# Optimization experiments

Measured on AMD Instinct MI355X. Metric: run time of the kernel, lower is better.

The kernel has to match this reference:

```python
import jax, jax.numpy as jnp
import numpy as np

NUM_PIECES = 32

def _conv(x, w, pad):
    # NCHW conv, stride 1
    return jax.lax.conv_general_dilated(x, w, (1, 1), [(pad, pad), (pad, pad)],
                                        dimension_numbers=('NCHW', 'OIHW', 'NCHW'))

def _bn(x, s, b):
    # eval-mode BatchNorm folded to per-channel affine (running mean/var folded into s,b)
    return x * s[None, :, None, None] + b[None, :, None, None]

def setup_inputs() -> dict:
    key = jax.random.key(0)
    ks = jax.random.split(key, 24)
    N, CIN, H, W = 1024, 13, 8, 8
    C = 64          # final conv channels
    S, NB = 7, 7    # stages, conv blocks per stage
    P = NUM_PIECES
    feat = jax.random.normal(ks[0], (N, CIN - 1, H, W), jnp.float32)
    ids = jax.random.randint(ks[1], (N, 1, H, W), 0, P + 1).astype(jnp.float32)
    x = jnp.concatenate([feat, ids], axis=1)  # last channel = piece ids
    n = jax.random.normal
    inp = {
        'x': x,
        'first_w': n(ks[2], (C - 1, CIN - 1, 7, 7), jnp.float32) * 0.05,
        'first_s': 1.0 + 0.1 * n(ks[3], (C - 1,), jnp.float32),
        'first_b': 0.05 * n(ks[4], (C - 1,), jnp.float32),
        'res_w': n(ks[5], (S, NB, C, C, 7, 7), jnp.float32) * 0.02,
        'res_s': 1.0 + 0.1 * n(ks[6], (S, NB, C), jnp.float32),
        'res_b': 0.05 * n(ks[7], (S, NB, C), jnp.float32),
        'last_w': n(ks[8], (S, C, C), jnp.float32) * 0.05,
        'last_s': 1.0 + 0.1 * n(ks[9], (S, C), jnp.float32),
        'last_b': 0.05 * n(ks[10], (S, C), jnp.float32),
        'pfc1_w': n(ks[11], (256, P * C), jnp.float32) * 0.02,
        'pfc1_b': jnp.zeros((256,), jnp.float32),
        'pfc2_w': n(ks[12], (1700, 256), jnp.float32) * 0.02,
        'pfc2_b': jnp.zeros((1700,), jnp.float32),
        'vconv_w': n(ks[13], (1, C, 1, 1), jnp.float32) * 0.05,
        'v_s': 1.0 + 0.1 * n(ks[14], (1,), jnp.float32),
        'v_b': 0.05 * n(ks[15], (1,), jnp.float32),
        'vfc1_w': n(ks[16], (256, H * W), jnp.float32) * 0.02,
        'vfc1_b': jnp.zeros((256,), jnp.float32),
        'vfc2_w': n(ks[17], (1, 256), jnp.float32) * 0.02,
        'vfc2_b': jnp.zeros((1,), jnp.float32),
    }
    return inp

def reference(x, first_w, first_s, first_b, res_w, res_s, res_b, last_w, last_s, last_b,
              pfc1_w, pfc1_b, pfc2_w, pfc2_b, vconv_w, v_s, v_b,
              vfc1_w, vfc1_b, vfc2_w, vfc2_b):
    N = x.shape[0]
    P = NUM_PIECES
    conv_in = x[:, :-1]           # (N, 12, 8, 8)
    ids_f = x[:, -1]              # (N, 8, 8) float piece ids
    ids = ids_f.astype(jnp.int32)
    h = jax.nn.relu(_bn(_conv(conv_in, first_w, 3), first_s, first_b))  # (N, 63, 8, 8)
    conv_feat = jnp.concatenate([h, ids_f[:, None]], axis=1)            # (N, 64, 8, 8)
    # --- fused piece-vector extraction (replaces batch x piece torch.where loop) ---
    ids_flat = ids.reshape(N, -1)                                       # (N, 64)
    match = ids_flat[:, None, :] == jnp.arange(1, P + 1, dtype=jnp.int32)[None, :, None]  # (N,P,64)
    idx = jnp.argmax(match, axis=-1)                                    # first occurrence, row-major
    present = match.any(-1)
    board_t = conv_feat.reshape(N, conv_feat.shape[1], -1).transpose(0, 2, 1)  # (N, 64pos, C)
    piece_vec = jnp.take_along_axis(board_t, idx[:, :, None], axis=1)          # (N, P, C)
    piece_vec = piece_vec * present[:, :, None].astype(piece_vec.dtype)
    pid_hist = [piece_vec[:, :, -1][:, None, :]]
    S, NB = res_w.shape[0], res_w.shape[1]
    for i in range(S):
        h = conv_feat
        for j in range(NB):
            h = jax.nn.relu(_bn(_conv(h, res_w[i, j], 3), res_s[i, j], res_b[i, j]))
        h = _bn(jnp.einsum('nchw,oc->nohw', h, last_w[i]), last_s[i], last_b[i])  # 1x1 conv
        conv_feat = jax.nn.relu(h + conv_feat)
        pid_hist.append(piece_vec[:, :, -1][:, None, :])
    piece_ids_out = jnp.concatenate(pid_hist, axis=1)  # (N, S+1, P)
    # policy head
    hid = jax.nn.relu(piece_vec.reshape(N, -1) @ pfc1_w.T + pfc1_b)
    policy = hid @ pfc2_w.T + pfc2_b                   # (N, 1700)
    # value head
    v = jax.nn.relu(_bn(_conv(conv_feat, vconv_w, 0), v_s, v_b)).reshape(N, -1)  # (N, 64)
    v = jax.nn.relu(v @ vfc1_w.T + vfc1_b)
    value = jnp.tanh(v @ vfc2_w.T + vfc2_b)            # (N, 1)
    return (policy, value, piece_ids_out)
```

## Files before the change

### kernel.cpp

```cpp
#include <hip/hip_runtime.h>

typedef __attribute__((ext_vector_type(8)))  short          bf16x8;
typedef __attribute__((ext_vector_type(16))) float          f32x16;
typedef __attribute__((ext_vector_type(4)))  unsigned int   uint4v;
typedef __attribute__((ext_vector_type(4)))  unsigned short ushort4v;
typedef __attribute__((ext_vector_type(4)))  float          float4v;

#define DEV static __device__ __forceinline__
#define MFMA32(A,B,C) __builtin_amdgcn_mfma_f32_32x32x16_bf16(A,B,C,0,0,0)

#define WRES_OFF 0u
#define FW_OFF   9863168u
#define P1_OFF   9913344u
#define P2_OFF   10437632u
#define ACT0_OFF 10896384u
#define PV_OFF   15090688u
#define HID_OFF  17187840u

#define VAL_OFF 1740800
#define PID_OFF 1741824

#define IMG_AREA 24576
#define SM_Z     98304
#define SM_BYTES 98432

DEV float bf2f(unsigned short u){ union { unsigned int i; float f; } v; v.i = ((unsigned int)u) << 16; return v.f; }
DEV unsigned short f2bf(float f){
  union { float f; unsigned int i; } v; v.f = f;
  unsigned int x = v.i;
  return (unsigned short)((x + 0x7fffu + ((x >> 16) & 1u)) >> 16);
}

__global__ void prep_res_k(const float* __restrict__ res_w, unsigned short* __restrict__ ws){
  __shared__ float buf[3136];
  int bx = blockIdx.x;
  int L = bx >> 6, o = bx & 63;
  const float* src = res_w + (size_t)bx * 3136;
  for (int e = threadIdx.x; e < 3136; e += 256) buf[e] = src[e];
  __syncthreads();
  unsigned short* dst = ws + WRES_OFF;
  int mt = o >> 5, lrow = o & 31;
  int tilebase = L*49 + L/7;
  for (int e = threadIdx.x; e < 3136; e += 256){
    int t = e >> 6, c = e & 63;
    int ks = c >> 4, hi = (c >> 3) & 1, j = c & 7;
    int lane = hi*32 + lrow;
    dst[(size_t)(tilebase + t)*4096 + ((ks*2 + mt)*64 + lane)*8 + j] = f2bf(buf[c*49 + t]);
  }
}

__global__ void prep_misc_k(const float* __restrict__ first_w, const float* __restrict__ last_w,
                            const float* __restrict__ pfc1_w, const float* __restrict__ pfc2_w,
                            unsigned short* __restrict__ ws){
  const int n_fw = 49*1024, n_lw = 28672, n_p1 = 524288, n_p2 = 458752;
  const int total = n_fw + n_lw + n_p1 + n_p2;
  for (int d = blockIdx.x*256 + threadIdx.x; d < total; d += gridDim.x*256){
    if (d < n_fw){
      int t = d >> 10, r = d & 1023;
      int mt = r >> 9, lane = (r >> 3) & 63, j = r & 7;
      int o = mt*32 + (lane & 31);
      int c = ((lane >> 5) << 3) + j;
      float v = (o < 63 && c < 12) ? first_w[(o*12 + c)*49 + t] : 0.f;
      ws[FW_OFF + d] = f2bf(v);
    } else if (d < n_fw + n_lw){
      int e = d - n_fw;
      int st = e >> 12, r = e & 4095;
      int f = r >> 9, lane = (r >> 3) & 63, j = r & 7;
      int ks = f >> 1, mt = f & 1;
      int o = mt*32 + (lane & 31);
      int c = ks*16 + ((lane >> 5) << 3) + j;
      ws[WRES_OFF + (size_t)(st*344 + 343)*4096 + r] = f2bf(last_w[st*4096 + o*64 + c]);
    } else if (d < n_fw + n_lw + n_p1){
      int e = d - n_fw - n_lw; ws[P1_OFF + e] = f2bf(pfc1_w[e]);
    } else {
      int e = d - n_fw - n_lw - n_p1;
      int row = e >> 8, k = e & 255;
      ws[P2_OFF + e] = f2bf(row < 1700 ? pfc2_w[row*256 + k] : 0.f);
    }
  }
}

DEV int baddr(int q, bool valid, int base, int hi16){
  return valid ? (base + (q << 7) + (hi16 ^ ((q & 7) << 4))) : (SM_Z + hi16);
}

#define LBAR() { asm volatile("s_waitcnt lgkmcnt(0)" ::: "memory"); \
                 __builtin_amdgcn_s_barrier(); \
                 asm volatile("" ::: "memory"); }

DEV void packst(unsigned char* sm, int scrb, int lane, int k, const f32x16& A){
  unsigned u[8];
  #pragma unroll
  for (int i = 0; i < 8; ++i)
    u[i] = (unsigned)f2bf(A[2*i]) | ((unsigned)f2bf(A[2*i+1]) << 16);
  uint4v* d = (uint4v*)(sm + scrb + k*2048 + lane*32);
  d[0] = uint4v{u[0],u[1],u[2],u[3]};
  d[1] = uint4v{u[4],u[5],u[6],u[7]};
}
DEV void ldadd(unsigned char* sm, int scrb, int lane, int k, f32x16& A){
  const uint4v* s = (const uint4v*)(sm + scrb + k*2048 + lane*32);
  uint4v a = s[0], b = s[1];
  #pragma unroll
  for (int i = 0; i < 4; ++i){
    A[2*i]   += bf2f((unsigned short)(a[i] & 0xffffu));
    A[2*i+1] += bf2f((unsigned short)(a[i] >> 16));
    A[8+2*i]   += bf2f((unsigned short)(b[i] & 0xffffu));
    A[8+2*i+1] += bf2f((unsigned short)(b[i] >> 16));
  }
}
#define STACC(scrb) { packst(sm,(scrb),lane,0,c00); packst(sm,(scrb),lane,1,c01); \
                      packst(sm,(scrb),lane,2,c10); packst(sm,(scrb),lane,3,c11); }
#define LDADD(scrb) { ldadd(sm,(scrb),lane,0,c00); ldadd(sm,(scrb),lane,1,c01); \
                      ldadd(sm,(scrb),lane,2,c10); ldadd(sm,(scrb),lane,3,c11); }

DEV void conv_epi(const f32x16& acc, int mt, int p, int wb, int hi,
                  unsigned char* smp, const float* sp, const float* bp){
  int swz = (p & 7) << 4; int rowb = wb + (p << 7);
  #pragma unroll
  for (int rg = 0; rg < 4; ++rg){
    int o0 = mt*32 + rg*8 + hi*4;
    unsigned short bb[4];
    #pragma unroll
    for (int e = 0; e < 4; ++e){
      float v = sp[o0+e]*acc[rg*4+e] + bp[o0+e];
      v = v > 0.f ? v : 0.f;
      bb[e] = f2bf(v);
    }
    int ob = mt*64 + rg*16 + hi*8;
    *(ushort4v*)(smp + rowb + (ob ^ swz)) = ushort4v{bb[0],bb[1],bb[2],bb[3]};
  }
}

DEV void res_epi(const f32x16& acc, int mt, int p, int rsb, int wb, int hi,
                 unsigned char* smp, const float* lsp, const float* lbp){
  int swz = (p & 7) << 4;
  int rrow = rsb + (p << 7), wrow = wb + (p << 7);
  #pragma unroll
  for (int rg = 0; rg < 4; ++rg){
    int o0 = mt*32 + rg*8 + hi*4;
    int ob = mt*64 + rg*16 + hi*8;
    ushort4v rv = *(const ushort4v*)(smp + rrow + (ob ^ swz));
    unsigned short bb[4];
    #pragma unroll
    for (int e = 0; e < 4; ++e){
      float v = lsp[o0+e]*acc[rg*4+e] + lbp[o0+e] + bf2f(rv[e]);
      v = v > 0.f ? v : 0.f;
      bb[e] = f2bf(v);
    }
    *(ushort4v*)(smp + wrow + (ob ^ swz)) = ushort4v{bb[0],bb[1],bb[2],bb[3]};
  }
}

DEV void first_epi(const f32x16& acc, int mt, int p, float idsv, int img, int wb, int hi,
                   unsigned char* smp, const float* fsp, const float* fbp,
                   unsigned short* act0){
  int swz = (p & 7) << 4; int rowb = wb + (p << 7);
  #pragma unroll
  for (int rg = 0; rg < 4; ++rg){
    int o0 = mt*32 + rg*8 + hi*4;
    unsigned short bb[4];
    #pragma unroll
    for (int e = 0; e < 4; ++e){
      int o = o0 + e;
      int oc = o < 63 ? o : 62;
      float v = fsp[oc]*acc[rg*4+e] + fbp[oc];
      v = v > 0.f ? v : 0.f;
      if (o == 63) v = idsv;
      bb[e] = f2bf(v);
    }
    int ob = mt*64 + rg*16 + hi*8;
    *(ushort4v*)(smp + rowb + (ob ^ swz)) = ushort4v{bb[0],bb[1],bb[2],bb[3]};
    *(ushort4v*)(act0 + (size_t)img*4096 + p*64 + o0) = ushort4v{bb[0],bb[1],bb[2],bb[3]};
  }
}

__global__ __launch_bounds__(1024, 4) __attribute__((amdgpu_waves_per_eu(4, 4)))
void tower_k(
    const float* __restrict__ x,
    const float* __restrict__ first_s, const float* __restrict__ first_b,
    const float* __restrict__ res_s,   const float* __restrict__ res_b,
    const float* __restrict__ last_s,  const float* __restrict__ last_b,
    const float* __restrict__ vconv_w, const float* __restrict__ v_s, const float* __restrict__ v_b,
    const float* __restrict__ vfc1_w,  const float* __restrict__ vfc1_b,
    const float* __restrict__ vfc2_w,  const float* __restrict__ vfc2_b,
    const unsigned short* __restrict__ ws_r, unsigned short* __restrict__ act0,
    float* __restrict__ value_out)
{
  __shared__ unsigned char sm[SM_BYTES];
  int tid = threadIdx.x, lane = tid & 63, wave = tid >> 6;
  int imgi = wave >> 2, tq = wave & 3;
  int img = blockIdx.x * 4 + imgi;

  for (int i = tid*16; i < SM_BYTES; i += 1024*16) *(float4v*)(sm + i) = float4v{0,0,0,0};
  __syncthreads();

  int col = lane & 31, hi = lane >> 5;
  int hi16 = hi << 4;
  int imgbase = imgi * IMG_AREA;
  int rS = imgbase, rA = imgbase + 8192, rB = imgbase + 16384;

  int p0 = col, p1 = 32 + col;
  int py0 = p0 >> 3, px0 = p0 & 7, py1 = p1 >> 3, px1 = p1 & 7;
  int t0 = tq*12, tend = (tq == 3) ? 49 : (t0 + 12);

  const float* xim = x + (size_t)img * 832;
  int xinb = rA;
  if (tq == 0){
    int q = (lane >> 3)*14 + (lane & 7) + 3;
    for (int c = 0; c < 12; ++c)
      *(unsigned short*)(sm + xinb + q*32 + c*2) = f2bf(xim[c*64 + lane]);
  }
  float ids0 = xim[768 + p0];
  float ids1 = xim[768 + p1];
  __syncthreads();

  {
    f32x16 c00 = {}, c01 = {}, c10 = {}, c11 = {};
    const unsigned short* fw = ws_r + FW_OFF;
    int qbx0 = py0*14 + px0, qbx1 = py1*14 + px1;
    for (int t = t0; t < tend; ++t){
      int dy = (t*37) >> 8, dx = t - dy*7;
      bf16x8 a0 = *(const bf16x8*)(fw + t*1024 +       lane*8);
      bf16x8 a1 = *(const bf16x8*)(fw + t*1024 + 512 + lane*8);
      bool v0 = (unsigned)(py0 + dy - 3) < 8u;
      bool v1 = (unsigned)(py1 + dy - 3) < 8u;
      int q0 = qbx0 + (dy-3)*14 + dx, q1 = qbx1 + (dy-3)*14 + dx;
      bf16x8 B0 = *(const bf16x8*)(sm + (v0 ? (xinb + q0*32 + hi16) : (SM_Z + hi16)));
      bf16x8 B1 = *(const bf16x8*)(sm + (v1 ? (xinb + q1*32 + hi16) : (SM_Z + hi16)));
      c00 = MFMA32(a0, B0, c00); c10 = MFMA32(a1, B0, c10);
      c01 = MFMA32(a0, B1, c01); c11 = MFMA32(a1, B1, c11);
    }
    int scr = rB;
    LBAR();
    if (tq == 3) STACC(scr);
    LBAR();
    if (tq == 2){ LDADD(scr); STACC(scr); }
    LBAR();
    if (tq == 1){ LDADD(scr); STACC(scr); }
    LBAR();
    if (tq == 0){
      LDADD(scr);
      first_epi(c00, 0, p0, ids0, img, rS, hi, sm, first_s, first_b, act0);
      first_epi(c10, 1, p0, ids0, img, rS, hi, sm, first_s, first_b, act0);
      first_epi(c01, 0, p1, ids1, img, rS, hi, sm, first_s, first_b, act0);
      first_epi(c11, 1, p1, ids1, img, rS, hi, sm, first_s, first_b, act0);
    }
    LBAR();
  }

  const unsigned short* wstream = ws_r + WRES_OFF;
  for (int st = 0; st < 7; ++st){
    int rd = rS, wr = rA;
    for (int j = 0; j < 7; ++j){
      int L = st*7 + j;
      const unsigned short* gwL = wstream + (size_t)(st*344 + j*49)*4096 + lane*8;
      f32x16 c00 = {}, c01 = {}, c10 = {}, c11 = {};
      for (int t = t0; t < tend; ++t){
        int dy = (t*37) >> 8, dx = t - dy*7;
        const unsigned short* wt = gwL + (size_t)t*4096;
        bf16x8 wv[8];
        #pragma unroll
        for (int f = 0; f < 8; ++f) wv[f] = *(const bf16x8*)(wt + f*512);
        int off = (dy - 3)*8 + (dx - 3);
        bool v0 = ((unsigned)(py0 + dy - 3) < 8u) && ((unsigned)(px0 + dx - 3) < 8u);
        bool v1 = ((unsigned)(py1 + dy - 3) < 8u) && ((unsigned)(px1 + dx - 3) < 8u);
        int b0 = baddr(p0 + off, v0, rd, hi16);
        int b1 = baddr(p1 + off, v1, rd, hi16);
        #pragma unroll
        for (int ks = 0; ks < 4; ++ks){
          bf16x8 B0 = *(const bf16x8*)(sm + (b0 ^ (ks << 5)));
          bf16x8 B1 = *(const bf16x8*)(sm + (b1 ^ (ks << 5)));
          c00 = MFMA32(wv[ks*2],   B0, c00);
          c10 = MFMA32(wv[ks*2+1], B0, c10);
          c01 = MFMA32(wv[ks*2],   B1, c01);
          c11 = MFMA32(wv[ks*2+1], B1, c11);
        }
      }
      int scr = (j == 0) ? rB : rd;
      LBAR();
      if (tq == 3) STACC(scr);
      LBAR();
      if (tq == 2){ LDADD(scr); STACC(scr); }
      LBAR();
      if (tq == 1){ LDADD(scr); STACC(scr); }
      LBAR();
      if (tq == 0){
        LDADD(scr);
        const float* sp = res_s + L*64;
        const float* bp = res_b + L*64;
        conv_epi(c00, 0, p0, wr, hi, sm, sp, bp);
        conv_epi(c10, 1, p0, wr, hi, sm, sp, bp);
        conv_epi(c01, 0, p1, wr, hi, sm, sp, bp);
        conv_epi(c11, 1, p1, wr, hi, sm, sp, bp);
      }
      LBAR();
      int nrd = wr; wr = (j == 0) ? rB : rd; rd = nrd;
    }
    if (tq == 0){
      const unsigned short* wt = wstream + (size_t)(st*344 + 343)*4096 + lane*8;
      bf16x8 wv[8];
      #pragma unroll
      for (int f = 0; f < 8; ++f) wv[f] = *(const bf16x8*)(wt + f*512);
      f32x16 c00 = {}, c01 = {}, c10 = {}, c11 = {};
      int b0 = baddr(p0, true, rd, hi16);
      int b1 = baddr(p1, true, rd, hi16);
      #pragma unroll
      for (int ks = 0; ks < 4; ++ks){
        bf16x8 B0 = *(const bf16x8*)(sm + (b0 ^ (ks << 5)));
        bf16x8 B1 = *(const bf16x8*)(sm + (b1 ^ (ks << 5)));
        c00 = MFMA32(wv[ks*2],   B0, c00);
        c10 = MFMA32(wv[ks*2+1], B0, c10);
        c01 = MFMA32(wv[ks*2],   B1, c01);
        c11 = MFMA32(wv[ks*2+1], B1, c11);
      }
      const float* lsp = last_s + st*64;
      const float* lbp = last_b + st*64;
      res_epi(c00, 0, p0, rS, rB, hi, sm, lsp, lbp);
      res_epi(c10, 1, p0, rS, rB, hi, sm, lsp, lbp);
      res_epi(c01, 0, p1, rS, rB, hi, sm, lsp, lbp);
      res_epi(c11, 1, p1, rS, rB, hi, sm, lsp, lbp);
    }
    LBAR();
    int ns = rB; rB = rS; rS = ns;
  }

  __syncthreads();
  if (tq == 0){
    float accv = 0.f;
    int rowa = rS + (lane << 7);
    int swz = (lane & 7) << 4;
    #pragma unroll
    for (int k = 0; k < 8; ++k){
      bf16x8 av = *(const bf16x8*)(sm + rowa + ((k*16) ^ swz));
      #pragma unroll
      for (int jj = 0; jj < 8; ++jj)
        accv += bf2f((unsigned short)av[jj]) * vconv_w[k*8 + jj];
    }
    float vv = v_s[0]*accv + v_b[0];
    vv = vv > 0.f ? vv : 0.f;
    float* vbuf = (float*)(sm + rA);
    vbuf[lane] = vv;
    asm volatile("s_waitcnt lgkmcnt(0)" ::: "memory");
    float hidv[4];
    #pragma unroll
    for (int it = 0; it < 4; ++it){
      int jj = it*64 + lane;
      float a = vfc1_b[jj];
      for (int k = 0; k < 64; k += 4){
        float4v v4 = *(const float4v*)(vbuf + k);
        a += vfc1_w[jj*64+k]*v4[0] + vfc1_w[jj*64+k+1]*v4[1]
           + vfc1_w[jj*64+k+2]*v4[2] + vfc1_w[jj*64+k+3]*v4[3];
      }
      hidv[it] = a > 0.f ? a : 0.f;
    }
    float tot = 0.f;
    #pragma unroll
    for (int it = 0; it < 4; ++it) tot += hidv[it]*vfc2_w[it*64 + lane];
    #pragma unroll
    for (int off = 32; off; off >>= 1) tot += __shfl_xor(tot, off);
    if (lane == 0) value_out[img] = tanhf(tot + vfc2_b[0]);
  }
}

__global__ __launch_bounds__(256) void gather_k(const unsigned short* __restrict__ act0,
                                                unsigned short* __restrict__ pvec,
                                                float* __restrict__ pid_out){
  int lane = threadIdx.x & 63, wave = threadIdx.x >> 6;
  int img = blockIdx.x*4 + wave;
  const unsigned short* arow = act0 + (size_t)img*4096;
  int myid = (int)bf2f(arow[lane*64 + 63]);
  int mypos = 0, mypres = 0;
  for (int p = 0; p < 32; ++p){
    unsigned long long m = __ballot(myid == (p+1));
    if (lane == p){ mypres = (m != 0ull); mypos = mypres ? (__ffsll(m) - 1) : 0; }
  }
  if (lane < 32){
    float v = mypres ? (float)(lane+1) : 0.f;
    #pragma unroll
    for (int s = 0; s < 8; ++s) pid_out[(size_t)img*256 + s*32 + lane] = v;
  }
  for (int p = 0; p < 32; ++p){
    int q  = __shfl(mypos, p);
    int pr = __shfl(mypres, p);
    unsigned short v = pr ? arow[q*64 + lane] : (unsigned short)0;
    pvec[(size_t)img*2048 + p*64 + lane] = v;
  }
}

__global__ __launch_bounds__(256) void fc1_k(const unsigned short* __restrict__ pvec,
                                             const unsigned short* __restrict__ w,
                                             const float* __restrict__ bias,
                                             unsigned short* __restrict__ hid){
  int lane = threadIdx.x & 63, wave = threadIdx.x >> 6;
  int col = lane & 31, hi = lane >> 5;
  int wm = wave >> 1, wn = wave & 1;
  int m0 = blockIdx.x*128 + wm*64;
  int n0 = blockIdx.y*128 + wn*64;
  f32x16 a00 = {}, a01 = {}, a10 = {}, a11 = {};
  for (int k = 0; k < 2048; k += 16){
    bf16x8 A0 = *(const bf16x8*)(pvec + (size_t)(m0+col)*2048    + k + hi*8);
    bf16x8 A1 = *(const bf16x8*)(pvec + (size_t)(m0+32+col)*2048 + k + hi*8);
    bf16x8 B0 = *(const bf16x8*)(w + (size_t)(n0+col)*2048    + k + hi*8);
    bf16x8 B1 = *(const bf16x8*)(w + (size_t)(n0+32+col)*2048 + k + hi*8);
    a00 = MFMA32(A0, B0, a00); a01 = MFMA32(A0, B1, a01);
    a10 = MFMA32(A1, B0, a10); a11 = MFMA32(A1, B1, a11);
  }
  #pragma unroll
  for (int mt = 0; mt < 2; ++mt)
    #pragma unroll
    for (int nt = 0; nt < 2; ++nt){
      const f32x16& acc = mt == 0 ? (nt == 0 ? a00 : a01) : (nt == 0 ? a10 : a11);
      int jcol = n0 + nt*32 + col;
      float bj = bias[jcol];
      #pragma unroll
      for (int rg = 0; rg < 4; ++rg)
        #pragma unroll
        for (int e = 0; e < 4; ++e){
          int n = m0 + mt*32 + rg*8 + hi*4 + e;
          float v = acc[rg*4+e] + bj; v = v > 0.f ? v : 0.f;
          hid[(size_t)n*256 + jcol] = f2bf(v);
        }
    }
}

__global__ __launch_bounds__(256) void fc2_k(const unsigned short* __restrict__ hid,
                                             const unsigned short* __restrict__ w,
                                             const float* __restrict__ bias,
                                             float* __restrict__ pol){
  int lane = threadIdx.x & 63, wave = threadIdx.x >> 6;
  int col = lane & 31, hi = lane >> 5;
  int wm = wave >> 1, wn = wave & 1;
  int m0 = blockIdx.x*128 + wm*64;
  int n0 = blockIdx.y*128 + wn*64;
  f32x16 a00 = {}, a01 = {}, a10 = {}, a11 = {};
  for (int k = 0; k < 256; k += 16){
    bf16x8 A0 = *(const bf16x8*)(hid + (size_t)(m0+col)*256    + k + hi*8);
    bf16x8 A1 = *(const bf16x8*)(hid + (size_t)(m0+32+col)*256 + k + hi*8);
    bf16x8 B0 = *(const bf16x8*)(w + (size_t)(n0+col)*256    + k + hi*8);
    bf16x8 B1 = *(const bf16x8*)(w + (size_t)(n0+32+col)*256 + k + hi*8);
    a00 = MFMA32(A0, B0, a00); a01 = MFMA32(A0, B1, a01);
    a10 = MFMA32(A1, B0, a10); a11 = MFMA32(A1, B1, a11);
  }
  #pragma unroll
  for (int mt = 0; mt < 2; ++mt)
    #pragma unroll
    for (int nt = 0; nt < 2; ++nt){
      const f32x16& acc = mt == 0 ? (nt == 0 ? a00 : a01) : (nt == 0 ? a10 : a11);
      int jcol = n0 + nt*32 + col;
      if (jcol < 1700){
        float bj = bias[jcol];
        #pragma unroll
        for (int rg = 0; rg < 4; ++rg)
          #pragma unroll
          for (int e = 0; e < 4; ++e){
            int n = m0 + mt*32 + rg*8 + hi*4 + e;
            pol[(size_t)n*1700 + jcol] = acc[rg*4+e] + bj;
          }
      }
    }
}

extern "C" void kernel_launch(void* const* d_in, const int* in_sizes, int n_in,
                              void* d_out, int out_size, void* d_ws, size_t ws_size,
                              hipStream_t stream){
  const float* x       = (const float*)d_in[0];
  const float* first_w = (const float*)d_in[1];
  const float* first_s = (const float*)d_in[2];
  const float* first_b = (const float*)d_in[3];
  const float* res_w   = (const float*)d_in[4];
  const float* res_s   = (const float*)d_in[5];
  const float* res_b   = (const float*)d_in[6];
  const float* last_w  = (const float*)d_in[7];
  const float* last_s  = (const float*)d_in[8];
  const float* last_b  = (const float*)d_in[9];
  const float* pfc1_w  = (const float*)d_in[10];
  const float* pfc1_b  = (const float*)d_in[11];
  const float* pfc2_w  = (const float*)d_in[12];
  const float* pfc2_b  = (const float*)d_in[13];
  const float* vconv_w = (const float*)d_in[14];
  const float* v_s     = (const float*)d_in[15];
  const float* v_b     = (const float*)d_in[16];
  const float* vfc1_w  = (const float*)d_in[17];
  const float* vfc1_b  = (const float*)d_in[18];
  const float* vfc2_w  = (const float*)d_in[19];
  const float* vfc2_b  = (const float*)d_in[20];
  unsigned short* ws = (unsigned short*)d_ws;
  float* out = (float*)d_out;

  prep_res_k <<<3136, 256, 0, stream>>>(res_w, ws);
  prep_misc_k<<<1024, 256, 0, stream>>>(first_w, last_w, pfc1_w, pfc2_w, ws);
  tower_k    <<<256, 1024, 0, stream>>>(x, first_s, first_b, res_s, res_b, last_s, last_b,
                                        vconv_w, v_s, v_b, vfc1_w, vfc1_b, vfc2_w, vfc2_b,
                                        ws, ws + ACT0_OFF, out + VAL_OFF);
  gather_k   <<<256, 256, 0, stream>>>(ws + ACT0_OFF, ws + PV_OFF, out + PID_OFF);
  fc1_k      <<<dim3(8, 2), 256, 0, stream>>>(ws + PV_OFF, ws + P1_OFF, pfc1_b, ws + HID_OFF);
  fc2_k      <<<dim3(8, 14), 256, 0, stream>>>(ws + HID_OFF, ws + P2_OFF, pfc2_b, out);
}
```

Before: 1.608 ms.

## Split residual conv work across waves by input-channel chunk instead of taps

The residual 7x7 convs previously split the 49 taps across four waves, and each wave loaded all four K-slices of the weights. Now each wave owns one 16-channel K-slice and loops over all 49 taps with a fully unrolled loop. The 1x1 conv is also split across all waves, with a shared REDUCE macro. Blocks shrink to 512 threads (2 images per block) with half the shared memory, and the grid doubles. This balances tap work evenly (49 is not divisible by 4) and removes the idle waves in the 1x1 stage. The cost is different occupancy behaviour and a larger unrolled loop that raises register pressure.

After: 2.661 ms. 1.66x slower.

```diff
diff --git a/kernel.cpp b/kernel.cpp
--- a/kernel.cpp
+++ b/kernel.cpp
@@ -21,8 +21,8 @@
 #define PID_OFF 1741824
 
 #define IMG_AREA 24576
-#define SM_Z     98304
-#define SM_BYTES 98432
+#define SM_Z     49152
+#define SM_BYTES 49280
 
 DEV float bf2f(unsigned short u){ union { unsigned int i; float f; } v; v.i = ((unsigned int)u) << 16; return v.f; }
 DEV unsigned short f2bf(float f){
@@ -80,10 +80,6 @@
   }
 }
 
-DEV int baddr(int q, bool valid, int base, int hi16){
-  return valid ? (base + (q << 7) + (hi16 ^ ((q & 7) << 4))) : (SM_Z + hi16);
-}
-
 #define LBAR() { asm volatile("s_waitcnt lgkmcnt(0)" ::: "memory"); \
                  __builtin_amdgcn_s_barrier(); \
                  asm volatile("" ::: "memory"); }
@@ -102,8 +98,8 @@
   uint4v a = s[0], b = s[1];
   #pragma unroll
   for (int i = 0; i < 4; ++i){
-    A[2*i]   += bf2f((unsigned short)(a[i] & 0xffffu));
-    A[2*i+1] += bf2f((unsigned short)(a[i] >> 16));
+    A[2*i]     += bf2f((unsigned short)(a[i] & 0xffffu));
+    A[2*i+1]   += bf2f((unsigned short)(a[i] >> 16));
     A[8+2*i]   += bf2f((unsigned short)(b[i] & 0xffffu));
     A[8+2*i+1] += bf2f((unsigned short)(b[i] >> 16));
   }
@@ -112,6 +108,11 @@
                       packst(sm,(scrb),lane,2,c10); packst(sm,(scrb),lane,3,c11); }
 #define LDADD(scrb) { ldadd(sm,(scrb),lane,0,c00); ldadd(sm,(scrb),lane,1,c01); \
                       ldadd(sm,(scrb),lane,2,c10); ldadd(sm,(scrb),lane,3,c11); }
+#define REDUCE(scrb) { \
+  LBAR(); if (kq == 3) STACC(scrb); \
+  LBAR(); if (kq == 2){ LDADD(scrb); STACC(scrb); } \
+  LBAR(); if (kq == 1){ LDADD(scrb); STACC(scrb); } \
+  LBAR(); if (kq == 0){ LDADD(scrb); } }
 
 DEV void conv_epi(const f32x16& acc, int mt, int p, int wb, int hi,
                   unsigned char* smp, const float* sp, const float* bp){
@@ -174,8 +175,7 @@
   }
 }
 
-__global__ __launch_bounds__(1024, 4) __attribute__((amdgpu_waves_per_eu(4, 4)))
-void tower_k(
+__global__ __launch_bounds__(512, 1) void tower_k(
     const float* __restrict__ x,
     const float* __restrict__ first_s, const float* __restrict__ first_b,
     const float* __restrict__ res_s,   const float* __restrict__ res_b,
@@ -188,24 +188,24 @@
 {
   __shared__ unsigned char sm[SM_BYTES];
   int tid = threadIdx.x, lane = tid & 63, wave = tid >> 6;
-  int imgi = wave >> 2, tq = wave & 3;
-  int img = blockIdx.x * 4 + imgi;
-
-  for (int i = tid*16; i < SM_BYTES; i += 1024*16) *(float4v*)(sm + i) = float4v{0,0,0,0};
+  int imgi = wave >> 2, kq = wave & 3;
+  int img = blockIdx.x * 2 + imgi;
+
+  for (int i = tid*16; i < SM_BYTES; i += 512*16) *(float4v*)(sm + i) = float4v{0,0,0,0};
   __syncthreads();
 
   int col = lane & 31, hi = lane >> 5;
   int hi16 = hi << 4;
+  int kqs  = kq << 5;
   int imgbase = imgi * IMG_AREA;
   int rS = imgbase, rA = imgbase + 8192, rB = imgbase + 16384;
 
   int p0 = col, p1 = 32 + col;
   int py0 = p0 >> 3, px0 = p0 & 7, py1 = p1 >> 3, px1 = p1 & 7;
-  int t0 = tq*12, tend = (tq == 3) ? 49 : (t0 + 12);
 
   const float* xim = x + (size_t)img * 832;
   int xinb = rA;
-  if (tq == 0){
+  if (kq == 0){
     int q = (lane >> 3)*14 + (lane & 7) + 3;
     for (int c = 0; c < 12; ++c)
       *(unsigned short*)(sm + xinb + q*32 + c*2) = f2bf(xim[c*64 + lane]);
@@ -215,11 +215,12 @@
   __syncthreads();
 
   {
+    int t0 = kq*12, tend = (kq == 3) ? 49 : (t0 + 12);
     f32x16 c00 = {}, c01 = {}, c10 = {}, c11 = {};
     const unsigned short* fw = ws_r + FW_OFF;
     int qbx0 = py0*14 + px0, qbx1 = py1*14 + px1;
     for (int t = t0; t < tend; ++t){
-      int dy = (t*37) >> 8, dx = t - dy*7;
+      int dy = t / 7, dx = t % 7;
       bf16x8 a0 = *(const bf16x8*)(fw + t*1024 +       lane*8);
       bf16x8 a1 = *(const bf16x8*)(fw + t*1024 + 512 + lane*8);
       bool v0 = (unsigned)(py0 + dy - 3) < 8u;
@@ -230,16 +231,8 @@
       c00 = MFMA32(a0, B0, c00); c10 = MFMA32(a1, B0, c10);
       c01 = MFMA32(a0, B1, c01); c11 = MFMA32(a1, B1, c11);
     }
-    int scr = rB;
-    LBAR();
-    if (tq == 3) STACC(scr);
-    LBAR();
-    if (tq == 2){ LDADD(scr); STACC(scr); }
-    LBAR();
-    if (tq == 1){ LDADD(scr); STACC(scr); }
-    LBAR();
-    if (tq == 0){
-      LDADD(scr);
+    REDUCE(rB);
+    if (kq == 0){
       first_epi(c00, 0, p0, ids0, img, rS, hi, sm, first_s, first_b, act0);
       first_epi(c10, 1, p0, ids0, img, rS, hi, sm, first_s, first_b, act0);
       first_epi(c01, 0, p1, ids1, img, rS, hi, sm, first_s, first_b, act0);
@@ -253,39 +246,28 @@
     int rd = rS, wr = rA;
     for (int j = 0; j < 7; ++j){
       int L = st*7 + j;
-      const unsigned short* gwL = wstream + (size_t)(st*344 + j*49)*4096 + lane*8;
+      const unsigned short* gwL = wstream + (size_t)(st*344 + j*49)*4096
+                                  + kq*1024 + lane*8;
       f32x16 c00 = {}, c01 = {}, c10 = {}, c11 = {};
-      for (int t = t0; t < tend; ++t){
-        int dy = (t*37) >> 8, dx = t - dy*7;
-        const unsigned short* wt = gwL + (size_t)t*4096;
-        bf16x8 wv[8];
-        #pragma unroll
-        for (int f = 0; f < 8; ++f) wv[f] = *(const bf16x8*)(wt + f*512);
-        int off = (dy - 3)*8 + (dx - 3);
+      #pragma unroll
+      for (int t = 0; t < 49; ++t){
+        const int dy = t / 7, dx = t % 7;
+        bf16x8 a0 = *(const bf16x8*)(gwL + (size_t)t*4096);
+        bf16x8 a1 = *(const bf16x8*)(gwL + (size_t)t*4096 + 512);
+        const int off = (dy - 3)*8 + (dx - 3);
         bool v0 = ((unsigned)(py0 + dy - 3) < 8u) && ((unsigned)(px0 + dx - 3) < 8u);
         bool v1 = ((unsigned)(py1 + dy - 3) < 8u) && ((unsigned)(px1 + dx - 3) < 8u);
-        int b0 = baddr(p0 + off, v0, rd, hi16);
-        int b1 = baddr(p1 + off, v1, rd, hi16);
-        #pragma unroll
-        for (int ks = 0; ks < 4; ++ks){
-          bf16x8 B0 = *(const bf16x8*)(sm + (b0 ^ (ks << 5)));
-          bf16x8 B1 = *(const bf16x8*)(sm + (b1 ^ (ks << 5)));
-          c00 = MFMA32(wv[ks*2],   B0, c00);
-          c10 = MFMA32(wv[ks*2+1], B0, c10);
-          c01 = MFMA32(wv[ks*2],   B1, c01);
-          c11 = MFMA32(wv[ks*2+1], B1, c11);
-        }
+        int pp0 = p0 + off, pp1 = p1 + off;
+        int b0 = (v0 ? (rd + (pp0 << 7) + (hi16 ^ ((pp0 & 7) << 4))) : (SM_Z + hi16)) ^ kqs;
+        int b1 = (v1 ? (rd + (pp1 << 7) + (hi16 ^ ((pp1 & 7) << 4))) : (SM_Z + hi16)) ^ kqs;
+        bf16x8 B0 = *(const bf16x8*)(sm + b0);
+        bf16x8 B1 = *(const bf16x8*)(sm + b1);
+        c00 = MFMA32(a0, B0, c00); c10 = MFMA32(a1, B0, c10);
+        c01 = MFMA32(a0, B1, c01); c11 = MFMA32(a1, B1, c11);
       }
       int scr = (j == 0) ? rB : rd;
-      LBAR();
-      if (tq == 3) STACC(scr);
-      LBAR();
-      if (tq == 2){ LDADD(scr); STACC(scr); }
-      LBAR();
-      if (tq == 1){ LDADD(scr); STACC(scr); }
-      LBAR();
-      if (tq == 0){
-        LDADD(scr);
+      REDUCE(scr);
+      if (kq == 0){
         const float* sp = res_s + L*64;
         const float* bp = res_b + L*64;
         conv_epi(c00, 0, p0, wr, hi, sm, sp, bp);
@@ -296,36 +278,33 @@
       LBAR();
       int nrd = wr; wr = (j == 0) ? rB : rd; rd = nrd;
     }
-    if (tq == 0){
-      const unsigned short* wt = wstream + (size_t)(st*344 + 343)*4096 + lane*8;
-      bf16x8 wv[8];
-      #pragma unroll
-      for (int f = 0; f < 8; ++f) wv[f] = *(const bf16x8*)(wt + f*512);
+    {
+      const unsigned short* wt = wstream + (size_t)(st*344 + 343)*4096 + kq*1024 + lane*8;
+      bf16x8 a0 = *(const bf16x8*)(wt);
+      bf16x8 a1 = *(const bf16x8*)(wt + 512);
       f32x16 c00 = {}, c01 = {}, c10 = {}, c11 = {};
-      int b0 = baddr(p0, true, rd, hi16);
-      int b1 = baddr(p1, true, rd, hi16);
-      #pragma unroll
-      for (int ks = 0; ks < 4; ++ks){
-        bf16x8 B0 = *(const bf16x8*)(sm + (b0 ^ (ks << 5)));
-        bf16x8 B1 = *(const bf16x8*)(sm + (b1 ^ (ks << 5)));
-        c00 = MFMA32(wv[ks*2],   B0, c00);
-        c10 = MFMA32(wv[ks*2+1], B0, c10);
-        c01 = MFMA32(wv[ks*2],   B1, c01);
-        c11 = MFMA32(wv[ks*2+1], B1, c11);
+      int b0 = (rd + (p0 << 7) + (hi16 ^ ((p0 & 7) << 4))) ^ kqs;
+      int b1 = (rd + (p1 << 7) + (hi16 ^ ((p1 & 7) << 4))) ^ kqs;
+      bf16x8 B0 = *(const bf16x8*)(sm + b0);
+      bf16x8 B1 = *(const bf16x8*)(sm + b1);
+      c00 = MFMA32(a0, B0, c00); c10 = MFMA32(a1, B0, c10);
+      c01 = MFMA32(a0, B1, c01); c11 = MFMA32(a1, B1, c11);
+      REDUCE(rd);
+      if (kq == 0){
+        const float* lsp = last_s + st*64;
+        const float* lbp = last_b + st*64;
+        res_epi(c00, 0, p0, rS, rB, hi, sm, lsp, lbp);
+        res_epi(c10, 1, p0, rS, rB, hi, sm, lsp, lbp);
+        res_epi(c01, 0, p1, rS, rB, hi, sm, lsp, lbp);
+        res_epi(c11, 1, p1, rS, rB, hi, sm, lsp, lbp);
       }
-      const float* lsp = last_s + st*64;
-      const float* lbp = last_b + st*64;
-      res_epi(c00, 0, p0, rS, rB, hi, sm, lsp, lbp);
-      res_epi(c10, 1, p0, rS, rB, hi, sm, lsp, lbp);
-      res_epi(c01, 0, p1, rS, rB, hi, sm, lsp, lbp);
-      res_epi(c11, 1, p1, rS, rB, hi, sm, lsp, lbp);
-    }
-    LBAR();
-    int ns = rB; rB = rS; rS = ns;
+      LBAR();
+      int ns = rB; rB = rS; rS = ns;
+    }
   }
 
   __syncthreads();
-  if (tq == 0){
+  if (kq == 0){
     float accv = 0.f;
     int rowa = rS + (lane << 7);
     int swz = (lane & 7) << 4;
@@ -489,9 +468,9 @@
 
   prep_res_k <<<3136, 256, 0, stream>>>(res_w, ws);
   prep_misc_k<<<1024, 256, 0, stream>>>(first_w, last_w, pfc1_w, pfc2_w, ws);
-  tower_k    <<<256, 1024, 0, stream>>>(x, first_s, first_b, res_s, res_b, last_s, last_b,
-                                        vconv_w, v_s, v_b, vfc1_w, vfc1_b, vfc2_w, vfc2_b,
-                                        ws, ws + ACT0_OFF, out + VAL_OFF);
+  tower_k    <<<512, 512, 0, stream>>>(x, first_s, first_b, res_s, res_b, last_s, last_b,
+                                       vconv_w, v_s, v_b, vfc1_w, vfc1_b, vfc2_w, vfc2_b,
+                                       ws, ws + ACT0_OFF, out + VAL_OFF);
   gather_k   <<<256, 256, 0, stream>>>(ws + ACT0_OFF, ws + PV_OFF, out + PID_OFF);
   fc1_k      <<<dim3(8, 2), 256, 0, stream>>>(ws + PV_OFF, ws + P1_OFF, pfc1_b, ws + HID_OFF);
   fc2_k      <<<dim3(8, 14), 256, 0, stream>>>(ws + HID_OFF, ws + P2_OFF, pfc2_b, out);
```

## Shrink tower blocks to two images and load weights per k-step

Applied to the files above, without the earlier changes.

The tower kernel now runs 512-thread blocks of two images each, launched as 512 blocks, and its shared memory is halved to match. Weight fragments are now loaded inside the k-step loop instead of being preloaded as eight vectors, which lowers register pressure, and the waves_per_eu attribute is dropped. This aims at better occupancy and finer scheduling across CUs, at the cost of exposing more global-load latency next to the MFMAs. A REDUCE macro factors out the cross-wave accumulator reduction.

Measured after the change: 1.555 ms. 1.03x faster.

```diff
diff --git a/kernel.cpp b/kernel.cpp
--- a/kernel.cpp
+++ b/kernel.cpp
@@ -21,8 +21,8 @@
 #define PID_OFF 1741824
 
 #define IMG_AREA 24576
-#define SM_Z     98304
-#define SM_BYTES 98432
+#define SM_Z     49152
+#define SM_BYTES 49280
 
 DEV float bf2f(unsigned short u){ union { unsigned int i; float f; } v; v.i = ((unsigned int)u) << 16; return v.f; }
 DEV unsigned short f2bf(float f){
@@ -102,8 +102,8 @@
   uint4v a = s[0], b = s[1];
   #pragma unroll
   for (int i = 0; i < 4; ++i){
-    A[2*i]   += bf2f((unsigned short)(a[i] & 0xffffu));
-    A[2*i+1] += bf2f((unsigned short)(a[i] >> 16));
+    A[2*i]     += bf2f((unsigned short)(a[i] & 0xffffu));
+    A[2*i+1]   += bf2f((unsigned short)(a[i] >> 16));
     A[8+2*i]   += bf2f((unsigned short)(b[i] & 0xffffu));
     A[8+2*i+1] += bf2f((unsigned short)(b[i] >> 16));
   }
@@ -112,6 +112,11 @@
                       packst(sm,(scrb),lane,2,c10); packst(sm,(scrb),lane,3,c11); }
 #define LDADD(scrb) { ldadd(sm,(scrb),lane,0,c00); ldadd(sm,(scrb),lane,1,c01); \
                       ldadd(sm,(scrb),lane,2,c10); ldadd(sm,(scrb),lane,3,c11); }
+#define REDUCE(scrb) { \
+  LBAR(); if (tq == 3) STACC(scrb); \
+  LBAR(); if (tq == 2){ LDADD(scrb); STACC(scrb); } \
+  LBAR(); if (tq == 1){ LDADD(scrb); STACC(scrb); } \
+  LBAR(); if (tq == 0){ LDADD(scrb); } }
 
 DEV void conv_epi(const f32x16& acc, int mt, int p, int wb, int hi,
                   unsigned char* smp, const float* sp, const float* bp){
@@ -174,8 +179,7 @@
   }
 }
 
-__global__ __launch_bounds__(1024, 4) __attribute__((amdgpu_waves_per_eu(4, 4)))
-void tower_k(
+__global__ __launch_bounds__(512, 4) void tower_k(
     const float* __restrict__ x,
     const float* __restrict__ first_s, const float* __restrict__ first_b,
     const float* __restrict__ res_s,   const float* __restrict__ res_b,
@@ -189,9 +193,9 @@
   __shared__ unsigned char sm[SM_BYTES];
   int tid = threadIdx.x, lane = tid & 63, wave = tid >> 6;
   int imgi = wave >> 2, tq = wave & 3;
-  int img = blockIdx.x * 4 + imgi;
-
-  for (int i = tid*16; i < SM_BYTES; i += 1024*16) *(float4v*)(sm + i) = float4v{0,0,0,0};
+  int img = blockIdx.x * 2 + imgi;
+
+  for (int i = tid*16; i < SM_BYTES; i += 512*16) *(float4v*)(sm + i) = float4v{0,0,0,0};
   __syncthreads();
 
   int col = lane & 31, hi = lane >> 5;
@@ -219,7 +223,7 @@
     const unsigned short* fw = ws_r + FW_OFF;
     int qbx0 = py0*14 + px0, qbx1 = py1*14 + px1;
     for (int t = t0; t < tend; ++t){
-      int dy = (t*37) >> 8, dx = t - dy*7;
+      int dy = t / 7, dx = t % 7;
       bf16x8 a0 = *(const bf16x8*)(fw + t*1024 +       lane*8);
       bf16x8 a1 = *(const bf16x8*)(fw + t*1024 + 512 + lane*8);
       bool v0 = (unsigned)(py0 + dy - 3) < 8u;
@@ -230,16 +234,8 @@
       c00 = MFMA32(a0, B0, c00); c10 = MFMA32(a1, B0, c10);
       c01 = MFMA32(a0, B1, c01); c11 = MFMA32(a1, B1, c11);
     }
-    int scr = rB;
-    LBAR();
-    if (tq == 3) STACC(scr);
-    LBAR();
-    if (tq == 2){ LDADD(scr); STACC(scr); }
-    LBAR();
-    if (tq == 1){ LDADD(scr); STACC(scr); }
-    LBAR();
+    REDUCE(rB);
     if (tq == 0){
-      LDADD(scr);
       first_epi(c00, 0, p0, ids0, img, rS, hi, sm, first_s, first_b, act0);
       first_epi(c10, 1, p0, ids0, img, rS, hi, sm, first_s, first_b, act0);
       first_epi(c01, 0, p1, ids1, img, rS, hi, sm, first_s, first_b, act0);
@@ -256,36 +252,26 @@
       const unsigned short* gwL = wstream + (size_t)(st*344 + j*49)*4096 + lane*8;
       f32x16 c00 = {}, c01 = {}, c10 = {}, c11 = {};
       for (int t = t0; t < tend; ++t){
-        int dy = (t*37) >> 8, dx = t - dy*7;
-        const unsigned short* wt = gwL + (size_t)t*4096;
-        bf16x8 wv[8];
-        #pragma unroll
-        for (int f = 0; f < 8; ++f) wv[f] = *(const bf16x8*)(wt + f*512);
+        int dy = t / 7, dx = t % 7;
         int off = (dy - 3)*8 + (dx - 3);
         bool v0 = ((unsigned)(py0 + dy - 3) < 8u) && ((unsigned)(px0 + dx - 3) < 8u);
         bool v1 = ((unsigned)(py1 + dy - 3) < 8u) && ((unsigned)(px1 + dx - 3) < 8u);
         int b0 = baddr(p0 + off, v0, rd, hi16);
         int b1 = baddr(p1 + off, v1, rd, hi16);
+        const unsigned short* wt = gwL + (size_t)t*4096;
         #pragma unroll
         for (int ks = 0; ks < 4; ++ks){
+          bf16x8 a0 = *(const bf16x8*)(wt + (ks*2    )*512);
+          bf16x8 a1 = *(const bf16x8*)(wt + (ks*2 + 1)*512);
           bf16x8 B0 = *(const bf16x8*)(sm + (b0 ^ (ks << 5)));
           bf16x8 B1 = *(const bf16x8*)(sm + (b1 ^ (ks << 5)));
-          c00 = MFMA32(wv[ks*2],   B0, c00);
-          c10 = MFMA32(wv[ks*2+1], B0, c10);
-          c01 = MFMA32(wv[ks*2],   B1, c01);
-          c11 = MFMA32(wv[ks*2+1], B1, c11);
+          c00 = MFMA32(a0, B0, c00); c10 = MFMA32(a1, B0, c10);
+          c01 = MFMA32(a0, B1, c01); c11 = MFMA32(a1, B1, c11);
         }
       }
       int scr = (j == 0) ? rB : rd;
-      LBAR();
-      if (tq == 3) STACC(scr);
-      LBAR();
-      if (tq == 2){ LDADD(scr); STACC(scr); }
-      LBAR();
-      if (tq == 1){ LDADD(scr); STACC(scr); }
-      LBAR();
+      REDUCE(scr);
       if (tq == 0){
-        LDADD(scr);
         const float* sp = res_s + L*64;
         const float* bp = res_b + L*64;
         conv_epi(c00, 0, p0, wr, hi, sm, sp, bp);
@@ -298,20 +284,17 @@
     }
     if (tq == 0){
       const unsigned short* wt = wstream + (size_t)(st*344 + 343)*4096 + lane*8;
-      bf16x8 wv[8];
-      #pragma unroll
-      for (int f = 0; f < 8; ++f) wv[f] = *(const bf16x8*)(wt + f*512);
       f32x16 c00 = {}, c01 = {}, c10 = {}, c11 = {};
       int b0 = baddr(p0, true, rd, hi16);
       int b1 = baddr(p1, true, rd, hi16);
       #pragma unroll
       for (int ks = 0; ks < 4; ++ks){
+        bf16x8 a0 = *(const bf16x8*)(wt + (ks*2    )*512);
+        bf16x8 a1 = *(const bf16x8*)(wt + (ks*2 + 1)*512);
         bf16x8 B0 = *(const bf16x8*)(sm + (b0 ^ (ks << 5)));
         bf16x8 B1 = *(const bf16x8*)(sm + (b1 ^ (ks << 5)));
-        c00 = MFMA32(wv[ks*2],   B0, c00);
-        c10 = MFMA32(wv[ks*2+1], B0, c10);
-        c01 = MFMA32(wv[ks*2],   B1, c01);
-        c11 = MFMA32(wv[ks*2+1], B1, c11);
+        c00 = MFMA32(a0, B0, c00); c10 = MFMA32(a1, B0, c10);
+        c01 = MFMA32(a0, B1, c01); c11 = MFMA32(a1, B1, c11);
       }
       const float* lsp = last_s + st*64;
       const float* lbp = last_b + st*64;
@@ -489,9 +472,9 @@
 
   prep_res_k <<<3136, 256, 0, stream>>>(res_w, ws);
   prep_misc_k<<<1024, 256, 0, stream>>>(first_w, last_w, pfc1_w, pfc2_w, ws);
-  tower_k    <<<256, 1024, 0, stream>>>(x, first_s, first_b, res_s, res_b, last_s, last_b,
-                                        vconv_w, v_s, v_b, vfc1_w, vfc1_b, vfc2_w, vfc2_b,
-                                        ws, ws + ACT0_OFF, out + VAL_OFF);
+  tower_k    <<<512, 512, 0, stream>>>(x, first_s, first_b, res_s, res_b, last_s, last_b,
+                                       vconv_w, v_s, v_b, vfc1_w, vfc1_b, vfc2_w, vfc2_b,
+                                       ws, ws + ACT0_OFF, out + VAL_OFF);
   gather_k   <<<256, 256, 0, stream>>>(ws + ACT0_OFF, ws + PV_OFF, out + PID_OFF);
   fc1_k      <<<dim3(8, 2), 256, 0, stream>>>(ws + PV_OFF, ws + P1_OFF, pfc1_b, ws + HID_OFF);
   fc2_k      <<<dim3(8, 14), 256, 0, stream>>>(ws + HID_OFF, ws + P2_OFF, pfc2_b, out);
```
